# Optimization experiments

Measured on AMD Instinct MI355X. Metric: run time of the kernel, lower is better.

Reference implementation:

```python
import jax, jax.numpy as jnp
import numpy as np

N = 50000      # nodes
E = 800000     # directed edges (avg degree 16)
IN = 96
H = 96
OUT = 96


def _gcn(x, W, b, src, dst, norm, n):
    # PyG GCNConv: h = x @ W; aggregate norm * h[src] at dst; add bias.
    h = x @ W                          # [N, H]
    msg = h[src] * norm[:, None]       # [E+N, H]
    out = jax.ops.segment_sum(msg, dst, num_segments=n)
    return out + b


def setup_inputs() -> dict:
    key = jax.random.key(0)
    ks = jax.random.split(key, 12)
    s = 1.0 / np.sqrt(IN)
    sh = 1.0 / np.sqrt(H)
    return {
        "x": jax.random.normal(ks[0], (N, IN), dtype=jnp.float32),
        "edge_index": jax.random.randint(ks[1], (2, E), 0, N, dtype=jnp.int32),
        "W_local": jax.random.uniform(ks[2], (IN, H), jnp.float32, -s, s),
        "b_local": jnp.zeros((H,), jnp.float32),
        "W_g1": jax.random.uniform(ks[3], (IN, H), jnp.float32, -s, s),
        "b_g1": jnp.zeros((H,), jnp.float32),
        "W_g2": jax.random.uniform(ks[4], (H, H), jnp.float32, -sh, sh),
        "b_g2": jnp.zeros((H,), jnp.float32),
        "W_fuse": jax.random.uniform(ks[5], (2 * H, OUT), jnp.float32, -1.0 / np.sqrt(2 * H), 1.0 / np.sqrt(2 * H)),
        "b_fuse": jnp.zeros((OUT,), jnp.float32),
    }


def reference(x, edge_index, W_local, b_local, W_g1, b_g1, W_g2, b_g2, W_fuse, b_fuse):
    n = x.shape[0]
    loops = jnp.arange(n, dtype=edge_index.dtype)
    src = jnp.concatenate([edge_index[0], loops])   # add self-loops (GCNConv default)
    dst = jnp.concatenate([edge_index[1], loops])
    deg = jax.ops.segment_sum(jnp.ones_like(dst, dtype=x.dtype), dst, num_segments=n)
    dis = jax.lax.rsqrt(jnp.maximum(deg, 1.0))      # deg >= 1 due to self-loops
    norm = dis[src] * dis[dst]                      # sym-normalized edge weights

    local = jax.nn.relu(_gcn(x, W_local, b_local, src, dst, norm, n))
    g = jax.nn.relu(_gcn(x, W_g1, b_g1, src, dst, norm, n))
    g = jax.nn.relu(_gcn(g, W_g2, b_g2, src, dst, norm, n))

    combined = jnp.concatenate([local, g], axis=-1)  # [N, 2H]
    return combined @ W_fuse + b_fuse                # [N, OUT]
```

## Files before the change

kernel.cpp:

```cpp
#include <hip/hip_runtime.h>

#define HDIM 96
#define LSTR 104

typedef __attribute__((ext_vector_type(8))) short bf16x8;
typedef __attribute__((ext_vector_type(4))) float f32x4;

#define LGKM0() do { asm volatile("s_waitcnt lgkmcnt(0)" ::: "memory"); \
                     __builtin_amdgcn_sched_barrier(0); } while (0)

__device__ __forceinline__ unsigned short bf16rne(float x) {
  const unsigned u = __float_as_uint(x);
  return (unsigned short)((u + 0x7fff + ((u >> 16) & 1)) >> 16);
}

__device__ __forceinline__ void split2(float x, unsigned short& hi, unsigned short& lo) {
  const unsigned u = __float_as_uint(x);
  hi = (unsigned short)(u >> 16);
  const float xhi = __uint_as_float(u & 0xffff0000u);
  lo = (unsigned short)(__float_as_uint(x - xhi) >> 16);
}

__global__ void zero_k(int* __restrict__ p, int n) {
  int i = blockIdx.x * blockDim.x + threadIdx.x;
  if (i < n) p[i] = 0;
}

__global__ void deg_rank_k(const int* __restrict__ dst, int* __restrict__ indeg,
                           int* __restrict__ rank, int e) {
  int i = blockIdx.x * blockDim.x + threadIdx.x;
  if (i < e) rank[i] = atomicAdd(&indeg[dst[i]], 1);
}

__device__ __forceinline__ int wave_incl_scan(int v, int lane) {
#pragma unroll
  for (int off = 1; off < 64; off <<= 1) {
    int t = __shfl_up(v, off, 64);
    if (lane >= off) v += t;
  }
  return v;
}

__global__ __launch_bounds__(1024) void scan_a_split_k(
    const int* __restrict__ indeg, int* __restrict__ bsum, int n, int nb,
    const float* __restrict__ W0, const float* __restrict__ W1,
    const float* __restrict__ W2, const float* __restrict__ W3,
    unsigned short* __restrict__ dH, unsigned short* __restrict__ dL) {
  const int tid = threadIdx.x;
  if (blockIdx.x >= nb) {
    const int t = (blockIdx.x - nb) * 1024 + tid;
    if (t < 5 * 9216) {
      const int tile = t / 9216, r = t % 9216;
      const int nn = r / 96, k = r % 96;
      const float* W = (tile == 0) ? W0 : (tile == 1) ? W1 : (tile == 2) ? W2 : W3;
      const int row = (tile == 4) ? 96 + k : k;
      unsigned short h, l;
      split2(W[row * 96 + nn], h, l);
      dH[t] = h;
      dL[t] = l;
    }
    return;
  }
  __shared__ int ws[16];
  const int i = blockIdx.x * 1024 + tid;
  int v = (i < n) ? indeg[i] : 0;
#pragma unroll
  for (int off = 32; off; off >>= 1) v += __shfl_down(v, off, 64);
  if ((tid & 63) == 0) ws[tid >> 6] = v;
  __syncthreads();
  if (tid < 16) {
    int s = ws[tid];
#pragma unroll
    for (int off = 8; off; off >>= 1) s += __shfl_down(s, off, 16);
    if (tid == 0) bsum[blockIdx.x] = s;
  }
}

__global__ __launch_bounds__(1024) void scan_b_k(const int* __restrict__ bsum,
                                                 int* __restrict__ bbase,
                                                 int* __restrict__ offsets, int nb, int n) {
  __shared__ int ws[16];
  const int tid = threadIdx.x, lane = tid & 63, w = tid >> 6;
  const int v = (tid < nb) ? bsum[tid] : 0;
  int incl = wave_incl_scan(v, lane);
  if (lane == 63) ws[w] = incl;
  __syncthreads();
  if (tid < 16) {
    int s = ws[tid];
#pragma unroll
    for (int off = 1; off < 16; off <<= 1) {
      int t = __shfl_up(s, off, 16);
      if (tid >= off) s += t;
    }
    ws[tid] = s;
  }
  __syncthreads();
  incl += (w > 0 ? ws[w - 1] : 0);
  if (tid < nb) bbase[tid] = incl - v;
  if (tid == 0) offsets[n] = ws[15];
}

__global__ __launch_bounds__(1024) void scan_c_k(const int* __restrict__ indeg,
                                                 const int* __restrict__ bbase,
                                                 int* __restrict__ offsets,
                                                 float* __restrict__ dis, int n) {
  __shared__ int ws[16];
  const int tid = threadIdx.x, lane = tid & 63, w = tid >> 6;
  const int i = blockIdx.x * 1024 + tid;
  const int v = (i < n) ? indeg[i] : 0;
  int incl = wave_incl_scan(v, lane);
  if (lane == 63) ws[w] = incl;
  __syncthreads();
  if (tid < 16) {
    int s = ws[tid];
#pragma unroll
    for (int off = 1; off < 16; off <<= 1) {
      int t = __shfl_up(s, off, 16);
      if (tid >= off) s += t;
    }
    ws[tid] = s;
  }
  __syncthreads();
  incl += (w > 0 ? ws[w - 1] : 0);
  if (i < n) {
    offsets[i] = bbase[blockIdx.x] + incl - v;
    dis[i] = rsqrtf((float)(1 + v));
  }
}

__global__ __launch_bounds__(256) void place_scale_k(
    const int* __restrict__ src, const int* __restrict__ dst,
    const int* __restrict__ rank, const int* __restrict__ offsets,
    int* __restrict__ csr_src, int e, int pb,
    const float* __restrict__ x, const float* __restrict__ dis,
    unsigned short* __restrict__ o, int n) {
  if (blockIdx.x < pb) {
    int i = blockIdx.x * 256 + threadIdx.x;
    if (i >= e) return;
    int d = dst[i];
    atomicExch(&csr_src[offsets[d] + rank[i]], src[i]);
  } else {
    int t = (blockIdx.x - pb) * 256 + threadIdx.x;
    if (t >= n * 24) return;
    const float d = dis[t / 24];
    float4 v = ((const float4*)x)[t];
    ushort4 h;
    h.x = bf16rne(v.x * d); h.y = bf16rne(v.y * d);
    h.z = bf16rne(v.z * d); h.w = bf16rne(v.w * d);
    ((ushort4*)o)[t] = h;
  }
}

__device__ __forceinline__ void acc8(float* a, uint4 p) {
  a[0] += __uint_as_float(p.x << 16);
  a[1] += __uint_as_float(p.x & 0xffff0000u);
  a[2] += __uint_as_float(p.y << 16);
  a[3] += __uint_as_float(p.y & 0xffff0000u);
  a[4] += __uint_as_float(p.z << 16);
  a[5] += __uint_as_float(p.z & 0xffff0000u);
  a[6] += __uint_as_float(p.w << 16);
  a[7] += __uint_as_float(p.w & 0xffff0000u);
}

__device__ __forceinline__ void gather_x4p(const int* __restrict__ csr,
                                           int i, int end,
                                           const unsigned short* __restrict__ hp,
                                           int quad, float a[3][8]) {
  const int q8 = 8 * quad;
  int s0 = 0, s1 = 0, s2 = 0, s3 = 0;
  if (i + 3 < end) { s0 = csr[i]; s1 = csr[i + 1]; s2 = csr[i + 2]; s3 = csr[i + 3]; }
  while (i + 3 < end) {
    const unsigned short* p0 = hp + (size_t)s0 * HDIM + q8;
    const unsigned short* p1 = hp + (size_t)s1 * HDIM + q8;
    const unsigned short* p2 = hp + (size_t)s2 * HDIM + q8;
    const unsigned short* p3 = hp + (size_t)s3 * HDIM + q8;
    const uint4 v00 = *(const uint4*)(p0), v01 = *(const uint4*)(p0 + 32), v02 = *(const uint4*)(p0 + 64);
    const uint4 v10 = *(const uint4*)(p1), v11 = *(const uint4*)(p1 + 32), v12 = *(const uint4*)(p1 + 64);
    const uint4 v20 = *(const uint4*)(p2), v21 = *(const uint4*)(p2 + 32), v22 = *(const uint4*)(p2 + 64);
    const uint4 v30 = *(const uint4*)(p3), v31 = *(const uint4*)(p3 + 32), v32 = *(const uint4*)(p3 + 64);
    i += 4;
    if (i + 3 < end) { s0 = csr[i]; s1 = csr[i + 1]; s2 = csr[i + 2]; s3 = csr[i + 3]; }
    acc8(a[0], v00); acc8(a[1], v01); acc8(a[2], v02);
    acc8(a[0], v10); acc8(a[1], v11); acc8(a[2], v12);
    acc8(a[0], v20); acc8(a[1], v21); acc8(a[2], v22);
    acc8(a[0], v30); acc8(a[1], v31); acc8(a[2], v32);
  }
  for (; i < end; i++) {
    const unsigned short* p = hp + (size_t)csr[i] * HDIM + q8;
    acc8(a[0], *(const uint4*)p);
    acc8(a[1], *(const uint4*)(p + 32));
    acc8(a[2], *(const uint4*)(p + 64));
  }
}

__device__ __forceinline__ void flush_tile(const unsigned short* TB,
                                           unsigned short* __restrict__ g,
                                           int row0w, int M, int lane) {
  const int rr = lane >> 2, sb = lane & 3;
  const int grow = row0w + rr;
#pragma unroll
  for (int j = 0; j < 3; j++) {
    const int slot = sb + 4 * j;
    const uint4 v = *(const uint4*)(&TB[rr * LSTR + slot * 8]);
    if (grow < M) *(uint4*)(&g[(size_t)grow * HDIM + slot * 8]) = v;
  }
}

template<bool DUAL, bool FUSE>
__global__ __launch_bounds__(256) void gat_gemm_k(
    const int* __restrict__ csr_src, const int* __restrict__ offsets,
    const float* __restrict__ dis, const unsigned short* __restrict__ hp,
    const unsigned short* __restrict__ WH0, const unsigned short* __restrict__ WL0,
    const float* __restrict__ b0,
    const unsigned short* __restrict__ WH1, const unsigned short* __restrict__ WL1,
    const float* __restrict__ b1,
    unsigned short* __restrict__ outH, unsigned short* __restrict__ outL,
    unsigned short* __restrict__ outMsg,
    const unsigned short* __restrict__ WH2, const unsigned short* __restrict__ WL2,
    const unsigned short* __restrict__ AH2, const unsigned short* __restrict__ AL2,
    const float* __restrict__ bF, float* __restrict__ fout, int M) {
  __shared__ __align__(16) unsigned short Wh[96 * LSTR], Wl[96 * LSTR];
  __shared__ __align__(16) unsigned short TBUF[4][16 * LSTR];
  const int t = threadIdx.x;
  const int lane = t & 63, wv = t >> 6;
  const int m = lane & 15, quad = lane >> 4;
  const int row0 = blockIdx.x * 64;
  const int node = row0 + 16 * wv + m;
  unsigned short* TB = TBUF[wv];

  for (int u = t; u < 1152; u += 256) {
    const int nn = u / 12, kq = u % 12;
    *(uint4*)(&Wh[nn * LSTR + 8 * kq]) = ((const uint4*)(WH0 + (size_t)nn * HDIM))[kq];
    *(uint4*)(&Wl[nn * LSTR + 8 * kq]) = ((const uint4*)(WL0 + (size_t)nn * HDIM))[kq];
  }

  float a[3][8];
#pragma unroll
  for (int c = 0; c < 3; c++)
#pragma unroll
    for (int jj = 0; jj < 8; jj++) a[c][jj] = 0.f;
  if (node < M) {
    const float dd = dis[node];
    const int beg = offsets[node];
    const int end = offsets[node + 1];
    const unsigned short* selfp = hp + (size_t)node * HDIM + 8 * quad;
    const uint4 sv0 = *(const uint4*)(selfp);
    const uint4 sv1 = *(const uint4*)(selfp + 32);
    const uint4 sv2 = *(const uint4*)(selfp + 64);
    gather_x4p(csr_src, beg, end, hp, quad, a);
    acc8(a[0], sv0); acc8(a[1], sv1); acc8(a[2], sv2);
#pragma unroll
    for (int c = 0; c < 3; c++)
#pragma unroll
      for (int jj = 0; jj < 8; jj++) a[c][jj] *= dd;
  }
  bf16x8 ah[3], al[3];
#pragma unroll
  for (int c = 0; c < 3; c++)
#pragma unroll
    for (int jj = 0; jj < 8; jj++) {
      unsigned short h, l;
      split2(a[c][jj], h, l);
      ah[c][jj] = (short)h;
      al[c][jj] = (short)l;
    }

  bf16x8 lh[3], ll[3];
  if (FUSE) {
#pragma unroll
    for (int kc = 0; kc < 3; kc++) { lh[kc] = (bf16x8){0,0,0,0,0,0,0,0}; ll[kc] = lh[kc]; }
    if (node < M) {
      const unsigned short* ph = AH2 + (size_t)node * HDIM + 8 * quad;
      const unsigned short* pl = AL2 + (size_t)node * HDIM + 8 * quad;
#pragma unroll
      for (int kc = 0; kc < 3; kc++) {
        lh[kc] = *(const bf16x8*)(ph + 32 * kc);
        ll[kc] = *(const bf16x8*)(pl + 32 * kc);
      }
    }
  }

  __syncthreads();

  f32x4 acc0[6];
#pragma unroll
  for (int c = 0; c < 6; c++) acc0[c] = (f32x4){0.f, 0.f, 0.f, 0.f};
#pragma unroll
  for (int kc = 0; kc < 3; kc++) {
    const int ko = 32 * kc + 8 * quad;
#pragma unroll
    for (int c = 0; c < 6; c++) {
      const bf16x8 wh = *(const bf16x8*)(&Wh[(16 * c + m) * LSTR + ko]);
      const bf16x8 wl = *(const bf16x8*)(&Wl[(16 * c + m) * LSTR + ko]);
      acc0[c] = __builtin_amdgcn_mfma_f32_16x16x32_bf16(ah[kc], wh, acc0[c], 0, 0, 0);
      acc0[c] = __builtin_amdgcn_mfma_f32_16x16x32_bf16(ah[kc], wl, acc0[c], 0, 0, 0);
      acc0[c] = __builtin_amdgcn_mfma_f32_16x16x32_bf16(al[kc], wh, acc0[c], 0, 0, 0);
    }
  }

  const int row0w = row0 + 16 * wv;

  if (!FUSE) {
#pragma unroll
    for (int c = 0; c < 6; c++) {
      const float bv = b0[16 * c + m];
#pragma unroll
      for (int r = 0; r < 4; r++) {
        const float v = fmaxf(acc0[c][r] + bv, 0.f);
        unsigned short h, l;
        split2(v, h, l);
        (void)l;
        TB[(4 * quad + r) * LSTR + 16 * c + m] = h;
      }
    }
    LGKM0();
    flush_tile(TB, outH, row0w, M, lane);
    LGKM0();
#pragma unroll
    for (int c = 0; c < 6; c++) {
      const float bv = b0[16 * c + m];
#pragma unroll
      for (int r = 0; r < 4; r++) {
        const float v = fmaxf(acc0[c][r] + bv, 0.f);
        unsigned short h, l;
        split2(v, h, l);
        (void)h;
        TB[(4 * quad + r) * LSTR + 16 * c + m] = l;
      }
    }
    LGKM0();
    flush_tile(TB, outL, row0w, M, lane);
    LGKM0();
  }

  if (DUAL) {
    __syncthreads();
    for (int u = t; u < 1152; u += 256) {
      const int nn = u / 12, kq = u % 12;
      *(uint4*)(&Wh[nn * LSTR + 8 * kq]) = ((const uint4*)(WH1 + (size_t)nn * HDIM))[kq];
      *(uint4*)(&Wl[nn * LSTR + 8 * kq]) = ((const uint4*)(WL1 + (size_t)nn * HDIM))[kq];
    }
    __syncthreads();
    f32x4 acc1[6];
#pragma unroll
    for (int c = 0; c < 6; c++) acc1[c] = (f32x4){0.f, 0.f, 0.f, 0.f};
#pragma unroll
    for (int kc = 0; kc < 3; kc++) {
      const int ko = 32 * kc + 8 * quad;
#pragma unroll
      for (int c = 0; c < 6; c++) {
        const bf16x8 wh = *(const bf16x8*)(&Wh[(16 * c + m) * LSTR + ko]);
        const bf16x8 wl = *(const bf16x8*)(&Wl[(16 * c + m) * LSTR + ko]);
        acc1[c] = __builtin_amdgcn_mfma_f32_16x16x32_bf16(ah[kc], wh, acc1[c], 0, 0, 0);
        acc1[c] = __builtin_amdgcn_mfma_f32_16x16x32_bf16(ah[kc], wl, acc1[c], 0, 0, 0);
        acc1[c] = __builtin_amdgcn_mfma_f32_16x16x32_bf16(al[kc], wh, acc1[c], 0, 0, 0);
      }
    }
    float dv[4];
#pragma unroll
    for (int r = 0; r < 4; r++) dv[r] = (row0w + 4 * quad + r < M) ? dis[row0w + 4 * quad + r] : 0.f;
#pragma unroll
    for (int c = 0; c < 6; c++) {
      const float bv = b1[16 * c + m];
#pragma unroll
      for (int r = 0; r < 4; r++)
        TB[(4 * quad + r) * LSTR + 16 * c + m] =
            bf16rne(fmaxf(acc1[c][r] + bv, 0.f) * dv[r]);
    }
    LGKM0();
    flush_tile(TB, outMsg, row0w, M, lane);
  }

  if (FUSE) {
    bf16x8 gh[3], gl[3];
#pragma unroll
    for (int c = 0; c < 6; c++) {
      const float bv = b0[16 * c + m];
#pragma unroll
      for (int r = 0; r < 4; r++) {
        const float v = fmaxf(acc0[c][r] + bv, 0.f);
        unsigned short h, l;
        split2(v, h, l);
        (void)l;
        TB[(4 * quad + r) * LSTR + 16 * c + m] = h;
      }
    }
    LGKM0();
#pragma unroll
    for (int kc = 0; kc < 3; kc++)
      gh[kc] = *(const bf16x8*)(&TB[m * LSTR + 32 * kc + 8 * quad]);
    LGKM0();
#pragma unroll
    for (int c = 0; c < 6; c++) {
      const float bv = b0[16 * c + m];
#pragma unroll
      for (int r = 0; r < 4; r++) {
        const float v = fmaxf(acc0[c][r] + bv, 0.f);
        unsigned short h, l;
        split2(v, h, l);
        (void)h;
        TB[(4 * quad + r) * LSTR + 16 * c + m] = l;
      }
    }
    LGKM0();
#pragma unroll
    for (int kc = 0; kc < 3; kc++)
      gl[kc] = *(const bf16x8*)(&TB[m * LSTR + 32 * kc + 8 * quad]);
    LGKM0();

    f32x4 accF[6];
#pragma unroll
    for (int c = 0; c < 6; c++) accF[c] = (f32x4){0.f, 0.f, 0.f, 0.f};

    __syncthreads();
    for (int u = t; u < 1152; u += 256) {
      const int nn = u / 12, kq = u % 12;
      *(uint4*)(&Wh[nn * LSTR + 8 * kq]) = ((const uint4*)(WH1 + (size_t)nn * HDIM))[kq];
      *(uint4*)(&Wl[nn * LSTR + 8 * kq]) = ((const uint4*)(WL1 + (size_t)nn * HDIM))[kq];
    }
    __syncthreads();
#pragma unroll
    for (int kc = 0; kc < 3; kc++) {
      const int ko = 32 * kc + 8 * quad;
#pragma unroll
      for (int c = 0; c < 6; c++) {
        const bf16x8 wh = *(const bf16x8*)(&Wh[(16 * c + m) * LSTR + ko]);
        const bf16x8 wl = *(const bf16x8*)(&Wl[(16 * c + m) * LSTR + ko]);
        accF[c] = __builtin_amdgcn_mfma_f32_16x16x32_bf16(lh[kc], wh, accF[c], 0, 0, 0);
        accF[c] = __builtin_amdgcn_mfma_f32_16x16x32_bf16(lh[kc], wl, accF[c], 0, 0, 0);
        accF[c] = __builtin_amdgcn_mfma_f32_16x16x32_bf16(ll[kc], wh, accF[c], 0, 0, 0);
      }
    }
    __syncthreads();
    for (int u = t; u < 1152; u += 256) {
      const int nn = u / 12, kq = u % 12;
      *(uint4*)(&Wh[nn * LSTR + 8 * kq]) = ((const uint4*)(WH2 + (size_t)nn * HDIM))[kq];
      *(uint4*)(&Wl[nn * LSTR + 8 * kq]) = ((const uint4*)(WL2 + (size_t)nn * HDIM))[kq];
    }
    __syncthreads();
#pragma unroll
    for (int kc = 0; kc < 3; kc++) {
      const int ko = 32 * kc + 8 * quad;
#pragma unroll
      for (int c = 0; c < 6; c++) {
        const bf16x8 wh = *(const bf16x8*)(&Wh[(16 * c + m) * LSTR + ko]);
        const bf16x8 wl = *(const bf16x8*)(&Wl[(16 * c + m) * LSTR + ko]);
        accF[c] = __builtin_amdgcn_mfma_f32_16x16x32_bf16(gh[kc], wh, accF[c], 0, 0, 0);
        accF[c] = __builtin_amdgcn_mfma_f32_16x16x32_bf16(gh[kc], wl, accF[c], 0, 0, 0);
        accF[c] = __builtin_amdgcn_mfma_f32_16x16x32_bf16(gl[kc], wh, accF[c], 0, 0, 0);
      }
    }

    float* TBf = (float*)TB;
    const int rr = lane >> 2, sb = lane & 3;
    const int grow = row0w + rr;
#pragma unroll
    for (int half = 0; half < 2; half++) {
#pragma unroll
      for (int c = 0; c < 3; c++) {
        const int cc = 3 * half + c;
        const float bv = bF[16 * cc + m];
#pragma unroll
        for (int r = 0; r < 4; r++)
          TBf[(4 * quad + r) * 52 + 16 * c + m] = accF[cc][r] + bv;
      }
      LGKM0();
#pragma unroll
      for (int j = 0; j < 3; j++) {
        const int slot = sb + 4 * j;
        const float4 v = *(const float4*)(&TBf[rr * 52 + slot * 4]);
        if (grow < M) *(float4*)(&fout[(size_t)grow * HDIM + half * 48 + slot * 4]) = v;
      }
      LGKM0();
    }
  }
}

extern "C" void kernel_launch(void* const* d_in, const int* in_sizes, int n_in,
                              void* d_out, int out_size, void* d_ws, size_t ws_size,
                              hipStream_t stream) {
  const float* x       = (const float*)d_in[0];
  const int*   edge    = (const int*)d_in[1];
  const float* W_local = (const float*)d_in[2];
  const float* b_local = (const float*)d_in[3];
  const float* W_g1    = (const float*)d_in[4];
  const float* b_g1    = (const float*)d_in[5];
  const float* W_g2    = (const float*)d_in[6];
  const float* b_g2    = (const float*)d_in[7];
  const float* W_fuse  = (const float*)d_in[8];
  const float* b_fuse  = (const float*)d_in[9];
  float* out = (float*)d_out;

  const int n = in_sizes[0] / HDIM;
  const int e = in_sizes[1] / 2;
  const int* src = edge;
  const int* dst = edge + e;
  const int nb = (n + 1023) / 1024;

  char* ws = (char*)d_ws;
  auto alloc = [&](size_t bytes) { char* p = ws; ws += (bytes + 255) & ~(size_t)255; return p; };
  int*   indeg   = (int*)alloc((size_t)n * 4);
  float* dis     = (float*)alloc((size_t)n * 4);
  int*   offsets = (int*)alloc((size_t)(n + 1) * 4);
  int*   bsum    = (int*)alloc((size_t)nb * 4);
  int*   bbase   = (int*)alloc((size_t)nb * 4);
  int*   rank    = (int*)alloc((size_t)e * 4);
  int*   csr_src = (int*)alloc((size_t)e * 4);
  const size_t mat16 = (size_t)n * HDIM * 2;
  unsigned short* msgX = (unsigned short*)alloc(mat16);
  unsigned short* msgG = (unsigned short*)alloc(mat16);
  unsigned short* locH = (unsigned short*)alloc(mat16);
  unsigned short* locL = (unsigned short*)alloc(mat16);
  unsigned short* wH   = (unsigned short*)alloc(5 * 9216 * 2);
  unsigned short* wL   = (unsigned short*)alloc(5 * 9216 * 2);

  zero_k<<<(n + 255) / 256, 256, 0, stream>>>(indeg, n);
  deg_rank_k<<<(e + 255) / 256, 256, 0, stream>>>(dst, indeg, rank, e);
  scan_a_split_k<<<nb + 45, 1024, 0, stream>>>(indeg, bsum, n, nb,
                                               W_local, W_g1, W_g2, W_fuse, wH, wL);
  scan_b_k<<<1, 1024, 0, stream>>>(bsum, bbase, offsets, nb, n);
  scan_c_k<<<nb, 1024, 0, stream>>>(indeg, bbase, offsets, dis, n);
  const int pb = (e + 255) / 256;
  const int sb = (n * 24 + 255) / 256;
  place_scale_k<<<pb + sb, 256, 0, stream>>>(src, dst, rank, offsets, csr_src, e, pb,
                                             x, dis, msgX, n);

  const int gb = (n + 63) / 64;

  gat_gemm_k<true, false><<<gb, 256, 0, stream>>>(csr_src, offsets, dis, msgX,
                                                  wH, wL, b_local,
                                                  wH + 9216, wL + 9216, b_g1,
                                                  locH, locL, msgG,
                                                  nullptr, nullptr, nullptr, nullptr,
                                                  nullptr, nullptr, n);
  gat_gemm_k<false, true><<<gb, 256, 0, stream>>>(csr_src, offsets, dis, msgG,
                                                  wH + 2 * 9216, wL + 2 * 9216, b_g2,
                                                  wH + 3 * 9216, wL + 3 * 9216, nullptr,
                                                  nullptr, nullptr, nullptr,
                                                  wH + 4 * 9216, wL + 4 * 9216,
                                                  locH, locL, b_fuse, out, n);
}
```

Measured before the change: 254.8 us.

## Fuse CSR preprocessing kernels into one persistent kernel with grid barriers

Replaces the six preprocessing launches (zero, degree/rank, three scan stages, placement/scale) with a single persistent kernel of 256 blocks that separates phases using a software grid barrier built on atomics. CSR placement now uses an atomic cursor per destination instead of a precomputed per-edge rank array, so the rank buffer and its extra read/write traffic go away. The aim is to remove launch gaps and tail effects between small kernels. In exchange it relies on all 256 blocks of 1024 threads being co-resident, or the barrier deadlocks. CSR order within a row becomes nondeterministic, which may change floating-point summation order.

Result: slower. 383.2 us (+50.4%).

```diff
diff --git a/kernel.cpp b/kernel.cpp
--- a/kernel.cpp
+++ b/kernel.cpp
@@ -21,17 +21,6 @@
   lo = (unsigned short)(__float_as_uint(x - xhi) >> 16);
 }
 
-__global__ void zero_k(int* __restrict__ p, int n) {
-  int i = blockIdx.x * blockDim.x + threadIdx.x;
-  if (i < n) p[i] = 0;
-}
-
-__global__ void deg_rank_k(const int* __restrict__ dst, int* __restrict__ indeg,
-                           int* __restrict__ rank, int e) {
-  int i = blockIdx.x * blockDim.x + threadIdx.x;
-  if (i < e) rank[i] = atomicAdd(&indeg[dst[i]], 1);
-}
-
 __device__ __forceinline__ int wave_incl_scan(int v, int lane) {
 #pragma unroll
   for (int off = 1; off < 64; off <<= 1) {
@@ -41,113 +30,120 @@
   return v;
 }
 
-__global__ __launch_bounds__(1024) void scan_a_split_k(
-    const int* __restrict__ indeg, int* __restrict__ bsum, int n, int nb,
+__device__ __forceinline__ void gsync(int* cnt, int* gen, int nb) {
+  __syncthreads();
+  if (threadIdx.x == 0) {
+    __threadfence();
+    const int g0 = __hip_atomic_load(gen, __ATOMIC_RELAXED, __HIP_MEMORY_SCOPE_AGENT);
+    const int a = __hip_atomic_fetch_add(cnt, 1, __ATOMIC_ACQ_REL, __HIP_MEMORY_SCOPE_AGENT);
+    if (a == nb - 1) {
+      __hip_atomic_store(cnt, 0, __ATOMIC_RELAXED, __HIP_MEMORY_SCOPE_AGENT);
+      __hip_atomic_fetch_add(gen, 1, __ATOMIC_RELEASE, __HIP_MEMORY_SCOPE_AGENT);
+    } else {
+      while (__hip_atomic_load(gen, __ATOMIC_ACQUIRE, __HIP_MEMORY_SCOPE_AGENT) == g0)
+        __builtin_amdgcn_s_sleep(2);
+    }
+  }
+  __syncthreads();
+}
+
+__global__ __launch_bounds__(1024, 4) void mega_pre_k(
+    const int* __restrict__ src, const int* __restrict__ dst, int e, int n,
     const float* __restrict__ W0, const float* __restrict__ W1,
     const float* __restrict__ W2, const float* __restrict__ W3,
-    unsigned short* __restrict__ dH, unsigned short* __restrict__ dL) {
-  const int tid = threadIdx.x;
-  if (blockIdx.x >= nb) {
-    const int t = (blockIdx.x - nb) * 1024 + tid;
-    if (t < 5 * 9216) {
-      const int tile = t / 9216, r = t % 9216;
-      const int nn = r / 96, k = r % 96;
-      const float* W = (tile == 0) ? W0 : (tile == 1) ? W1 : (tile == 2) ? W2 : W3;
-      const int row = (tile == 4) ? 96 + k : k;
-      unsigned short h, l;
-      split2(W[row * 96 + nn], h, l);
-      dH[t] = h;
-      dL[t] = l;
-    }
-    return;
-  }
+    unsigned short* __restrict__ wH, unsigned short* __restrict__ wL,
+    int* __restrict__ indeg, int* __restrict__ offsets,
+    int* __restrict__ cursor, float* __restrict__ dis,
+    int* __restrict__ bsum, int* __restrict__ csr_src,
+    const float* __restrict__ x, unsigned short* __restrict__ msgX,
+    int* __restrict__ bar_cnt, int* __restrict__ bar_gen) {
   __shared__ int ws[16];
-  const int i = blockIdx.x * 1024 + tid;
-  int v = (i < n) ? indeg[i] : 0;
-#pragma unroll
-  for (int off = 32; off; off >>= 1) v += __shfl_down(v, off, 64);
-  if ((tid & 63) == 0) ws[tid >> 6] = v;
-  __syncthreads();
-  if (tid < 16) {
-    int s = ws[tid];
-#pragma unroll
-    for (int off = 8; off; off >>= 1) s += __shfl_down(s, off, 16);
-    if (tid == 0) bsum[blockIdx.x] = s;
-  }
-}
-
-__global__ __launch_bounds__(1024) void scan_b_k(const int* __restrict__ bsum,
-                                                 int* __restrict__ bbase,
-                                                 int* __restrict__ offsets, int nb, int n) {
-  __shared__ int ws[16];
-  const int tid = threadIdx.x, lane = tid & 63, w = tid >> 6;
-  const int v = (tid < nb) ? bsum[tid] : 0;
-  int incl = wave_incl_scan(v, lane);
-  if (lane == 63) ws[w] = incl;
-  __syncthreads();
-  if (tid < 16) {
-    int s = ws[tid];
-#pragma unroll
-    for (int off = 1; off < 16; off <<= 1) {
-      int t = __shfl_up(s, off, 16);
-      if (tid >= off) s += t;
-    }
-    ws[tid] = s;
-  }
-  __syncthreads();
-  incl += (w > 0 ? ws[w - 1] : 0);
-  if (tid < nb) bbase[tid] = incl - v;
-  if (tid == 0) offsets[n] = ws[15];
-}
-
-__global__ __launch_bounds__(1024) void scan_c_k(const int* __restrict__ indeg,
-                                                 const int* __restrict__ bbase,
-                                                 int* __restrict__ offsets,
-                                                 float* __restrict__ dis, int n) {
-  __shared__ int ws[16];
-  const int tid = threadIdx.x, lane = tid & 63, w = tid >> 6;
-  const int i = blockIdx.x * 1024 + tid;
-  const int v = (i < n) ? indeg[i] : 0;
-  int incl = wave_incl_scan(v, lane);
-  if (lane == 63) ws[w] = incl;
-  __syncthreads();
-  if (tid < 16) {
-    int s = ws[tid];
-#pragma unroll
-    for (int off = 1; off < 16; off <<= 1) {
-      int t = __shfl_up(s, off, 16);
-      if (tid >= off) s += t;
-    }
-    ws[tid] = s;
-  }
-  __syncthreads();
-  incl += (w > 0 ? ws[w - 1] : 0);
-  if (i < n) {
-    offsets[i] = bbase[blockIdx.x] + incl - v;
-    dis[i] = rsqrtf((float)(1 + v));
-  }
-}
-
-__global__ __launch_bounds__(256) void place_scale_k(
-    const int* __restrict__ src, const int* __restrict__ dst,
-    const int* __restrict__ rank, const int* __restrict__ offsets,
-    int* __restrict__ csr_src, int e, int pb,
-    const float* __restrict__ x, const float* __restrict__ dis,
-    unsigned short* __restrict__ o, int n) {
-  if (blockIdx.x < pb) {
-    int i = blockIdx.x * 256 + threadIdx.x;
-    if (i >= e) return;
-    int d = dst[i];
-    atomicExch(&csr_src[offsets[d] + rank[i]], src[i]);
-  } else {
-    int t = (blockIdx.x - pb) * 256 + threadIdx.x;
-    if (t >= n * 24) return;
-    const float d = dis[t / 24];
-    float4 v = ((const float4*)x)[t];
+  __shared__ int warr[64];
+  const int tid = threadIdx.x, bid = blockIdx.x;
+  const int nb = gridDim.x;
+  const int NT = nb * 1024;
+  const int g = bid * 1024 + tid;
+
+  for (int i = g; i < n; i += NT) indeg[i] = 0;
+  for (int t = g; t < 5 * 9216; t += NT) {
+    const int tile = t / 9216, r = t % 9216;
+    const int nn = r / 96, k = r % 96;
+    const float* W = (tile == 0) ? W0 : (tile == 1) ? W1 : (tile == 2) ? W2 : W3;
+    const int row = (tile == 4) ? 96 + k : k;
+    unsigned short h, l;
+    split2(W[row * 96 + nn], h, l);
+    wH[t] = h;
+    wL[t] = l;
+  }
+  gsync(bar_cnt, bar_gen, nb);
+
+  for (int i = g; i < e; i += NT) atomicAdd(&indeg[dst[i]], 1);
+  gsync(bar_cnt, bar_gen, nb);
+
+  const int nch = (n + 1023) / 1024;
+  if (bid < nch) {
+    const int i = bid * 1024 + tid;
+    int v = (i < n) ? indeg[i] : 0;
+#pragma unroll
+    for (int off = 32; off; off >>= 1) v += __shfl_down(v, off, 64);
+    if ((tid & 63) == 0) ws[tid >> 6] = v;
+    __syncthreads();
+    if (tid < 16) {
+      int s = ws[tid];
+#pragma unroll
+      for (int off = 8; off; off >>= 1) s += __shfl_down(s, off, 16);
+      if (tid == 0) bsum[bid] = s;
+    }
+  }
+  gsync(bar_cnt, bar_gen, nb);
+
+  if (bid < nch) {
+    if (tid < 64) {
+      const int v = (tid < nch) ? bsum[tid] : 0;
+      warr[tid] = wave_incl_scan(v, tid);
+    }
+    __syncthreads();
+    const int bbase = (bid > 0) ? warr[bid - 1] : 0;
+    if (bid == 0 && tid == 0) offsets[n] = warr[nch - 1];
+    const int i = bid * 1024 + tid;
+    const int lane = tid & 63, w = tid >> 6;
+    const int v = (i < n) ? indeg[i] : 0;
+    int incl = wave_incl_scan(v, lane);
+    if (lane == 63) ws[w] = incl;
+    __syncthreads();
+    if (tid < 16) {
+      int s = ws[tid];
+#pragma unroll
+      for (int off = 1; off < 16; off <<= 1) {
+        int t2 = __shfl_up(s, off, 16);
+        if (tid >= off) s += t2;
+      }
+      ws[tid] = s;
+    }
+    __syncthreads();
+    incl += (w > 0 ? ws[w - 1] : 0);
+    if (i < n) {
+      const int off = bbase + incl - v;
+      offsets[i] = off;
+      cursor[i] = off;
+      dis[i] = rsqrtf((float)(1 + v));
+    }
+  }
+  gsync(bar_cnt, bar_gen, nb);
+
+  for (int i = g; i < e; i += NT) {
+    const int d = dst[i];
+    const int slot = atomicAdd(&cursor[d], 1);
+    csr_src[slot] = src[i];
+  }
+  const int nq = n * 24;
+  for (int t2 = g; t2 < nq; t2 += NT) {
+    const float dd = dis[t2 / 24];
+    const float4 v = ((const float4*)x)[t2];
     ushort4 h;
-    h.x = bf16rne(v.x * d); h.y = bf16rne(v.y * d);
-    h.z = bf16rne(v.z * d); h.w = bf16rne(v.w * d);
-    ((ushort4*)o)[t] = h;
+    h.x = bf16rne(v.x * dd); h.y = bf16rne(v.y * dd);
+    h.z = bf16rne(v.z * dd); h.w = bf16rne(v.w * dd);
+    ((ushort4*)msgX)[t2] = h;
   }
 }
 
@@ -495,16 +491,15 @@
   const int e = in_sizes[1] / 2;
   const int* src = edge;
   const int* dst = edge + e;
-  const int nb = (n + 1023) / 1024;
+  const int nch = (n + 1023) / 1024;
 
   char* ws = (char*)d_ws;
   auto alloc = [&](size_t bytes) { char* p = ws; ws += (bytes + 255) & ~(size_t)255; return p; };
   int*   indeg   = (int*)alloc((size_t)n * 4);
   float* dis     = (float*)alloc((size_t)n * 4);
   int*   offsets = (int*)alloc((size_t)(n + 1) * 4);
-  int*   bsum    = (int*)alloc((size_t)nb * 4);
-  int*   bbase   = (int*)alloc((size_t)nb * 4);
-  int*   rank    = (int*)alloc((size_t)e * 4);
+  int*   cursor  = (int*)alloc((size_t)n * 4);
+  int*   bsum    = (int*)alloc((size_t)nch * 4);
   int*   csr_src = (int*)alloc((size_t)e * 4);
   const size_t mat16 = (size_t)n * HDIM * 2;
   unsigned short* msgX = (unsigned short*)alloc(mat16);
@@ -513,17 +508,14 @@
   unsigned short* locL = (unsigned short*)alloc(mat16);
   unsigned short* wH   = (unsigned short*)alloc(5 * 9216 * 2);
   unsigned short* wL   = (unsigned short*)alloc(5 * 9216 * 2);
-
-  zero_k<<<(n + 255) / 256, 256, 0, stream>>>(indeg, n);
-  deg_rank_k<<<(e + 255) / 256, 256, 0, stream>>>(dst, indeg, rank, e);
-  scan_a_split_k<<<nb + 45, 1024, 0, stream>>>(indeg, bsum, n, nb,
-                                               W_local, W_g1, W_g2, W_fuse, wH, wL);
-  scan_b_k<<<1, 1024, 0, stream>>>(bsum, bbase, offsets, nb, n);
-  scan_c_k<<<nb, 1024, 0, stream>>>(indeg, bbase, offsets, dis, n);
-  const int pb = (e + 255) / 256;
-  const int sb = (n * 24 + 255) / 256;
-  place_scale_k<<<pb + sb, 256, 0, stream>>>(src, dst, rank, offsets, csr_src, e, pb,
-                                             x, dis, msgX, n);
+  int*   bar     = (int*)alloc(2 * 4);
+
+  hipMemsetAsync(bar, 0, 8, stream);
+
+  mega_pre_k<<<256, 1024, 0, stream>>>(src, dst, e, n,
+                                       W_local, W_g1, W_g2, W_fuse, wH, wL,
+                                       indeg, offsets, cursor, dis, bsum, csr_src,
+                                       x, msgX, bar, bar + 1);
 
   const int gb = (n + 63) / 64;
 
```
